# Kernel tuning notes

Hardware: AMD Instinct MI355X
Metric: run time of the kernel (lower is better)

Reference implementation:

```python
import jax, jax.numpy as jnp
import numpy as np

B, C, W, H, HEADS = 8, 512, 32, 32, 8
DH = C // HEADS  # 64
N = W * H        # 1024


def setup_inputs() -> dict:
    key = jax.random.key(0)
    ks = jax.random.split(key, 10)
    s = 1.0 / np.sqrt(C)
    return {
        "x": jax.random.normal(ks[0], (B, C, W, H), jnp.float32),
        "d": jax.random.normal(ks[1], (B, C, W, H), jnp.float32),
        "Wq": jax.random.normal(ks[2], (C, C), jnp.float32) * s,
        "bq": jnp.zeros((C,), jnp.float32),
        "Wk": jax.random.normal(ks[3], (C, C), jnp.float32) * s,
        "bk": jnp.zeros((C,), jnp.float32),
        "Wv": jax.random.normal(ks[4], (C, C), jnp.float32) * s,
        "bv": jnp.zeros((C,), jnp.float32),
        "rel_h": jax.random.normal(ks[5], (1, HEADS, DH, 1, H), jnp.float32),
        "rel_w": jax.random.normal(ks[6], (1, HEADS, DH, W, 1), jnp.float32),
    }


def reference(x, d, Wq, bq, Wk, bk, Wv, bv, rel_h, rel_w):
    b, c, w, h = x.shape
    heads = rel_h.shape[1]
    dh = c // heads
    n = w * h

    def proj(t, Wt, bt):
        # 1x1 conv == per-pixel channel matmul; reshape to [B, heads, dh, N]
        y = jnp.einsum('bchw,oc->bohw', t, Wt) + bt[None, :, None, None]
        return y.reshape(b, heads, dh, n)

    q = proj(x, Wq, bq)
    k = proj(d, Wk, bk)
    v = proj(d, Wv, bv)

    # content-content: q^T k -> [B, h, N, N]
    cc = jnp.einsum('bhdn,bhdm->bhnm', q, k)
    # content-position: (rel_h + rel_w) broadcast -> [1, h, dh, N], then pos^T @ q
    pos = (rel_h + rel_w).reshape(heads, dh, n)
    cp = jnp.einsum('hdm,bhdn->bhmn', pos, q)

    attn = jax.nn.softmax(cc + cp, axis=-1)  # [B, h, N, N]
    # out = v @ attn^T : out[b,h,d,i] = sum_j v[b,h,d,j] * attn[b,h,i,j]
    out = jnp.einsum('bhdj,bhij->bhdi', v, attn)
    return out.reshape(b, c, w, h)
```

## Files before the change

kernel.cpp:

```cpp
#include <hip/hip_runtime.h>

typedef unsigned short u16;
typedef _Float16 f16x8 __attribute__((ext_vector_type(8)));
typedef __fp16 hf16x2 __attribute__((ext_vector_type(2)));
typedef float f32x4 __attribute__((ext_vector_type(4)));
typedef float f32x16 __attribute__((ext_vector_type(16)));
typedef unsigned uint2v __attribute__((ext_vector_type(2)));

#define NB 8
#define NC 512
#define NHD 8
#define DH 64
#define NN 1024
#define LOG2E 1.4426950408889634f

__device__ __forceinline__ u16 f2h(float f) {
    union { _Float16 h; u16 u; } v; v.h = (_Float16)f;
    return v.u;
}

__global__ __launch_bounds__(256) void k_prep(
    const float* __restrict__ x, const float* __restrict__ d,
    const float* __restrict__ Wq, const float* __restrict__ Wk, const float* __restrict__ Wv,
    const float* __restrict__ relh, const float* __restrict__ relw,
    u16* __restrict__ xt, u16* __restrict__ dt,
    u16* __restrict__ wq, u16* __restrict__ wk, u16* __restrict__ wv,
    u16* __restrict__ ps) {
    __shared__ float tile[64][65];
    int id = blockIdx.x, t = threadIdx.x;
    if (id < 2048) {
        int nb = (id & 15) * 64;
        int cb = ((id >> 4) & 7) * 64;
        int z = id >> 7;
        int b = z & 7;
        const float* src = (z >> 3) ? d : x;
        u16* ot = (z >> 3) ? dt : xt;
        {
            int crow = t >> 2, n0 = (t & 3) * 16;
            const float* g = src + ((size_t)(b * NC + cb + crow)) * NN + nb + n0;
#pragma unroll
            for (int k = 0; k < 16; k += 4) {
                float4 v = *(const float4*)(g + k);
                tile[crow][n0 + k + 0] = v.x;
                tile[crow][n0 + k + 1] = v.y;
                tile[crow][n0 + k + 2] = v.z;
                tile[crow][n0 + k + 3] = v.w;
            }
        }
        __syncthreads();
        {
            int nrow = t >> 2, c0 = (t & 3) * 16;
            union { u16 s[16]; uint4 v[2]; } uh;
#pragma unroll
            for (int k = 0; k < 16; ++k) uh.s[k] = f2h(tile[c0 + k][nrow]);
            size_t oidx = ((size_t)(b * NN + nb + nrow)) * NC + cb + c0;
            *(uint4*)(ot + oidx)     = uh.v[0];
            *(uint4*)(ot + oidx + 8) = uh.v[1];
        }
    } else if (id < 2816) {
        int j = id - 2048;
        int m = j >> 8;
        int blk = j & 255;
        const float* src = (m == 0) ? Wq : (m == 1) ? Wk : Wv;
        u16* dst = (m == 0) ? wq : (m == 1) ? wk : wv;
        int i = (blk * 256 + t) * 4;
        float4 v = *(const float4*)(src + i);
        union { u16 s[4]; uint2 u2; } r;
        r.s[0] = f2h(v.x); r.s[1] = f2h(v.y); r.s[2] = f2h(v.z); r.s[3] = f2h(v.w);
        *(uint2*)(dst + i) = r.u2;
    } else {
        int idx = (id - 2816) * 256 + t;
        int dd = idx & 63;
        int i  = (idx >> 6) & 1023;
        int h  = idx >> 16;
        float f = relh[(h * 64 + dd) * 32 + (i & 31)] + relw[(h * 64 + dd) * 32 + (i >> 5)];
        ps[(h * 1024 + i) * 64 + dd] = f2h(f);
    }
}

__global__ __launch_bounds__(256) void k_proj(
    const u16* __restrict__ xt, const u16* __restrict__ dt,
    const u16* __restrict__ wq, const u16* __restrict__ wk, const u16* __restrict__ wv,
    const float* __restrict__ bq, const float* __restrict__ bk, const float* __restrict__ bv,
    u16* __restrict__ qt_o, u16* __restrict__ kt_o, u16* __restrict__ v_o) {
    __shared__ u16 Asm[128 * 32];
    __shared__ u16 Bsm[128 * 32];

    int p = blockIdx.z % 3;
    int b = blockIdx.z / 3;
    const u16 *Ap, *Bp;
    const float* bias;
    u16* Oq;
    if (p == 0)      { Ap = wq; Bp = xt; bias = bq; Oq = qt_o; }
    else if (p == 1) { Ap = wk; Bp = dt; bias = bk; Oq = kt_o; }
    else             { Ap = wv; Bp = dt; bias = bv; Oq = v_o; }
    Bp += (size_t)b * NN * NC;
    float oscale = (p == 0) ? LOG2E : 1.0f;

    int obase = blockIdx.x * 128;
    int nbase = blockIdx.y * 128;
    int t = threadIdx.x, wave = t >> 6, quad = (t & 63) >> 4, l15 = t & 15;
    int wr = (wave >> 1) * 64, wc = (wave & 1) * 64;

    f32x4 acc[4][4];
#pragma unroll
    for (int fo = 0; fo < 4; ++fo)
#pragma unroll
        for (int fn = 0; fn < 4; ++fn)
#pragma unroll
            for (int r = 0; r < 4; ++r) acc[fo][fn][r] = 0.f;

    for (int kk = 0; kk < NC; kk += 32) {
        __syncthreads();
#pragma unroll
        for (int u = 0; u < 2; ++u) {
            int c = u * 256 + t;
            int row = c >> 2, part = c & 3;
            __builtin_amdgcn_global_load_lds(
                (const __attribute__((address_space(1))) void*)(Ap + (size_t)(obase + row) * NC + kk + part * 8),
                (__attribute__((address_space(3))) void*)(Asm + (size_t)(u * 256 + wave * 64) * 8), 16, 0, 0);
            __builtin_amdgcn_global_load_lds(
                (const __attribute__((address_space(1))) void*)(Bp + (size_t)(nbase + row) * NC + kk + part * 8),
                (__attribute__((address_space(3))) void*)(Bsm + (size_t)(u * 256 + wave * 64) * 8), 16, 0, 0);
        }
        __syncthreads();

        f16x8 af[4], bfr[4];
#pragma unroll
        for (int fo = 0; fo < 4; ++fo) af[fo] = *(const f16x8*)&Asm[(wr + fo * 16 + l15) * 32 + quad * 8];
#pragma unroll
        for (int fn = 0; fn < 4; ++fn) bfr[fn] = *(const f16x8*)&Bsm[(wc + fn * 16 + l15) * 32 + quad * 8];
#pragma unroll
        for (int fo = 0; fo < 4; ++fo)
#pragma unroll
            for (int fn = 0; fn < 4; ++fn)
                acc[fo][fn] = __builtin_amdgcn_mfma_f32_16x16x32_f16(af[fo], bfr[fn], acc[fo][fn], 0, 0, 0);
    }

#pragma unroll
    for (int fo = 0; fo < 4; ++fo) {
#pragma unroll
        for (int fn = 0; fn < 4; ++fn) {
            int o0 = obase + wr + fo * 16 + quad * 4;
            int n = nbase + wc + fn * 16 + l15;
            if (p < 2) {
                union { u16 s[4]; uint2 v2; } uh;
#pragma unroll
                for (int r = 0; r < 4; ++r) uh.s[r] = f2h((acc[fo][fn][r] + bias[o0 + r]) * oscale);
                int head = o0 >> 6, dd0 = o0 & 63;
                size_t idx = (((size_t)(b * NHD + head) * NN) + n) * DH + dd0;
                *(uint2*)&Oq[idx] = uh.v2;
            } else {
#pragma unroll
                for (int r = 0; r < 4; ++r) {
                    int o = o0 + r;
                    int head = o >> 6, dd = o & 63;
                    Oq[((size_t)(b * NHD + head) * DH + dd) * NN + n] = f2h(acc[fo][fn][r] + bias[o]);
                }
            }
        }
    }
}

__global__ __launch_bounds__(256, 2) void k_attn(
    const u16* __restrict__ qt, const u16* __restrict__ kt,
    const u16* __restrict__ v_, const u16* __restrict__ pos,
    float* __restrict__ out) {
    __shared__ u16 Bs[128 * 128];
    __shared__ u16 Vt[64 * 128];

    int n = blockIdx.x;
    int g = n & 63;
    int ib = n >> 6;
    int head = g & 7, b = g >> 3;

    int t = threadIdx.x, ws = t >> 6, lane = t & 63, h = lane >> 5, l31 = lane & 31;
    size_t bh = (size_t)(b * NHD + head);
    const u16* qb = qt + bh * NN * DH;
    const u16* kb = kt + bh * NN * DH;
    const u16* vb = v_ + bh * DH * NN;
    const u16* pb = pos + (size_t)head * NN * DH;
    int i0 = ib * 128;
    int iglob = i0 + ws * 32 + l31;

    f16x8 qf[8];
#pragma unroll
    for (int ks = 0; ks < 4; ++ks) qf[ks] = *(const f16x8*)&qb[(size_t)iglob * DH + ks * 16 + h * 8];
#pragma unroll
    for (int ks = 4; ks < 8; ++ks) qf[ks] = *(const f16x8*)&pb[(size_t)iglob * DH + (ks - 4) * 16 + h * 8];

    f32x16 oacc[2];
#pragma unroll
    for (int df = 0; df < 2; ++df)
#pragma unroll
        for (int r = 0; r < 16; ++r) oacc[df][r] = 0.f;
    float m_ = -__builtin_inff(), l_ = 0.f;
    int swz = l31 & 7;

    for (int jc = 0; jc < NN; jc += 128) {
        __syncthreads();
#pragma unroll
        for (int u = 0; u < 8; ++u) {
            int c = u * 256 + t;
            int row = c >> 4, c16 = c & 15;
            int gch = c16 ^ (row & 7);
            const u16* src = (gch < 8) ? &kb[(size_t)(jc + row) * DH + gch * 8]
                                       : &qb[(size_t)(jc + row) * DH + (gch - 8) * 8];
            __builtin_amdgcn_global_load_lds(
                (const __attribute__((address_space(1))) void*)src,
                (__attribute__((address_space(3))) void*)(Bs + (u * 256 + ws * 64) * 8), 16, 0, 0);
        }
#pragma unroll
        for (int u = 0; u < 4; ++u) {
            int c = u * 256 + t;
            int row = c >> 4, c16 = c & 15;
            int gch = c16 ^ (row & 7);
            __builtin_amdgcn_global_load_lds(
                (const __attribute__((address_space(1))) void*)&vb[(size_t)row * NN + jc + gch * 8],
                (__attribute__((address_space(3))) void*)(Vt + (u * 256 + ws * 64) * 8), 16, 0, 0);
        }
        __syncthreads();

        f32x16 sacc[4];
#pragma unroll
        for (int jf = 0; jf < 4; ++jf)
#pragma unroll
            for (int r = 0; r < 16; ++r) sacc[jf][r] = 0.f;
        __builtin_amdgcn_s_setprio(1);
#pragma unroll
        for (int jf = 0; jf < 4; ++jf)
#pragma unroll
            for (int ks = 0; ks < 8; ++ks) {
                f16x8 af = *(const f16x8*)&Bs[(jf * 32 + l31) * 128 + ((ks * 2 + h) ^ swz) * 8];
                sacc[jf] = __builtin_amdgcn_mfma_f32_32x32x16_f16(af, qf[ks], sacc[jf], 0, 0, 0);
            }
        __builtin_amdgcn_s_setprio(0);

        float mj[4];
#pragma unroll
        for (int jf = 0; jf < 4; ++jf) {
            float a = fmaxf(fmaxf(sacc[jf][0], sacc[jf][1]), sacc[jf][2]);
            a = fmaxf(fmaxf(a, sacc[jf][3]), sacc[jf][4]);
            a = fmaxf(fmaxf(a, sacc[jf][5]), sacc[jf][6]);
            a = fmaxf(fmaxf(a, sacc[jf][7]), sacc[jf][8]);
            a = fmaxf(fmaxf(a, sacc[jf][9]), sacc[jf][10]);
            a = fmaxf(fmaxf(a, sacc[jf][11]), sacc[jf][12]);
            a = fmaxf(fmaxf(a, sacc[jf][13]), sacc[jf][14]);
            mj[jf] = fmaxf(a, sacc[jf][15]);
        }
        float mloc = fmaxf(fmaxf(mj[0], mj[1]), fmaxf(mj[2], mj[3]));
        mloc = fmaxf(mloc, __shfl_xor(mloc, 32));
        if (__any(mloc - m_ > 8.f)) {
            float mnew = fmaxf(m_, mloc);
            float alpha = __builtin_amdgcn_exp2f(m_ - mnew);
            m_ = mnew;
#pragma unroll
            for (int df = 0; df < 2; ++df)
#pragma unroll
                for (int r = 0; r < 16; ++r) oacc[df][r] *= alpha;
            l_ *= alpha;
        }
        float ls[4];
#pragma unroll
        for (int jf = 0; jf < 4; ++jf) {
            float s = 0.f;
#pragma unroll
            for (int r = 0; r < 16; ++r) {
                float pv = __builtin_amdgcn_exp2f(sacc[jf][r] - m_);
                sacc[jf][r] = pv;
                s += pv;
            }
            ls[jf] = s;
        }
        float lsum = (ls[0] + ls[1]) + (ls[2] + ls[3]);
        lsum += __shfl_xor(lsum, 32);
        l_ += lsum;

        __builtin_amdgcn_s_setprio(1);
#pragma unroll
        for (int jw = 0; jw < 8; ++jw) {
            int jf = jw >> 1, r0 = (jw & 1) * 8;
            union { hf16x2 v; unsigned u; } a0, a1, b0, b1;
            a0.v = __builtin_amdgcn_cvt_pkrtz(sacc[jf][r0 + 0], sacc[jf][r0 + 1]);
            a1.v = __builtin_amdgcn_cvt_pkrtz(sacc[jf][r0 + 2], sacc[jf][r0 + 3]);
            b0.v = __builtin_amdgcn_cvt_pkrtz(sacc[jf][r0 + 4], sacc[jf][r0 + 5]);
            b1.v = __builtin_amdgcn_cvt_pkrtz(sacc[jf][r0 + 6], sacc[jf][r0 + 7]);
            uint2v s0 = __builtin_amdgcn_permlane32_swap(a0.u, b0.u, false, false);
            uint2v s1 = __builtin_amdgcn_permlane32_swap(a1.u, b1.u, false, false);
            union { unsigned w[4]; f16x8 f; } pf;
            pf.w[0] = s0.x;
            pf.w[1] = s1.x;
            pf.w[2] = s0.y;
            pf.w[3] = s1.y;
#pragma unroll
            for (int df = 0; df < 2; ++df) {
                f16x8 vf = *(const f16x8*)&Vt[(df * 32 + l31) * 128 + ((jw * 2 + h) ^ swz) * 8];
                oacc[df] = __builtin_amdgcn_mfma_f32_32x32x16_f16(vf, pf.f, oacc[df], 0, 0, 0);
            }
        }
        __builtin_amdgcn_s_setprio(0);
    }

    float li = 1.0f / l_;
#pragma unroll
    for (int df = 0; df < 2; ++df)
#pragma unroll
        for (int r = 0; r < 16; ++r) {
            int dd = df * 32 + (r & 3) + 8 * (r >> 2) + 4 * h;
            out[((size_t)(b * NC) + head * DH + dd) * NN + i0 + ws * 32 + l31] = oacc[df][r] * li;
        }
}

#define SXT  (8u * 1024u * 512u * 2u)
#define SW   (512u * 512u * 2u)
#define SQT  SXT
#define SPOS (8u * 1024u * 64u * 2u)

#define OFF_XT   (0u)
#define OFF_DT   (OFF_XT + SXT)
#define OFF_WQ   (OFF_DT + SXT)
#define OFF_WK   (OFF_WQ + SW)
#define OFF_WV   (OFF_WK + SW)
#define OFF_QT   (OFF_WV + SW)
#define OFF_KT   (OFF_QT + SQT)
#define OFF_V    (OFF_KT + SQT)
#define OFF_POS  (OFF_V + SQT)

extern "C" void kernel_launch(void* const* d_in, const int* in_sizes, int n_in,
                              void* d_out, int out_size, void* d_ws, size_t ws_size,
                              hipStream_t stream) {
    const float* x   = (const float*)d_in[0];
    const float* d   = (const float*)d_in[1];
    const float* Wq  = (const float*)d_in[2];
    const float* bq  = (const float*)d_in[3];
    const float* Wk  = (const float*)d_in[4];
    const float* bk  = (const float*)d_in[5];
    const float* Wv  = (const float*)d_in[6];
    const float* bv  = (const float*)d_in[7];
    const float* rh  = (const float*)d_in[8];
    const float* rw  = (const float*)d_in[9];

    char* ws = (char*)d_ws;
    u16* xt = (u16*)(ws + OFF_XT);
    u16* dt = (u16*)(ws + OFF_DT);
    u16* wq = (u16*)(ws + OFF_WQ);
    u16* wk = (u16*)(ws + OFF_WK);
    u16* wv = (u16*)(ws + OFF_WV);
    u16* qt = (u16*)(ws + OFF_QT);
    u16* kt = (u16*)(ws + OFF_KT);
    u16* v_ = (u16*)(ws + OFF_V);
    u16* ps = (u16*)(ws + OFF_POS);

    k_prep<<<4864, 256, 0, stream>>>(x, d, Wq, Wk, Wv, rh, rw, xt, dt, wq, wk, wv, ps);
    k_proj<<<dim3(4, 8, 24), 256, 0, stream>>>(xt, dt, wq, wk, wv, bq, bk, bv, qt, kt, v_);
    k_attn<<<512, 256, 0, stream>>>(qt, kt, v_, ps, (float*)d_out);
}
```

Baseline: 164.8 us.

## Double-buffer LDS tiles in projection and attention kernels

Both the projection GEMM and the attention kernel now use two LDS buffers. Each iteration issues the async global-to-LDS loads for the next tile before computing on the current one, and synchronises once at the end of the iteration instead of twice. To keep the LDS budget unchanged, the attention key/value chunk shrinks from 128 to 64 columns, which doubles the number of softmax and rescale steps per row block. The goal is to hide global load latency behind MFMA work, at the cost of more loop overhead and more online-softmax bookkeeping.

```diff
diff --git a/kernel.cpp b/kernel.cpp
--- a/kernel.cpp
+++ b/kernel.cpp
@@ -83,8 +83,8 @@
     const u16* __restrict__ wq, const u16* __restrict__ wk, const u16* __restrict__ wv,
     const float* __restrict__ bq, const float* __restrict__ bk, const float* __restrict__ bv,
     u16* __restrict__ qt_o, u16* __restrict__ kt_o, u16* __restrict__ v_o) {
-    __shared__ u16 Asm[128 * 32];
-    __shared__ u16 Bsm[128 * 32];
+    __shared__ u16 Asm[2][128 * 32];
+    __shared__ u16 Bsm[2][128 * 32];
 
     int p = blockIdx.z % 3;
     int b = blockIdx.z / 3;
@@ -110,31 +110,39 @@
 #pragma unroll
             for (int r = 0; r < 4; ++r) acc[fo][fn][r] = 0.f;
 
-    for (int kk = 0; kk < NC; kk += 32) {
-        __syncthreads();
+    auto stage = [&](int kk, int buf) {
 #pragma unroll
         for (int u = 0; u < 2; ++u) {
             int c = u * 256 + t;
             int row = c >> 2, part = c & 3;
             __builtin_amdgcn_global_load_lds(
                 (const __attribute__((address_space(1))) void*)(Ap + (size_t)(obase + row) * NC + kk + part * 8),
-                (__attribute__((address_space(3))) void*)(Asm + (size_t)(u * 256 + wave * 64) * 8), 16, 0, 0);
+                (__attribute__((address_space(3))) void*)(&Asm[buf][0] + (size_t)(u * 256 + wave * 64) * 8), 16, 0, 0);
             __builtin_amdgcn_global_load_lds(
                 (const __attribute__((address_space(1))) void*)(Bp + (size_t)(nbase + row) * NC + kk + part * 8),
-                (__attribute__((address_space(3))) void*)(Bsm + (size_t)(u * 256 + wave * 64) * 8), 16, 0, 0);
-        }
-        __syncthreads();
+                (__attribute__((address_space(3))) void*)(&Bsm[buf][0] + (size_t)(u * 256 + wave * 64) * 8), 16, 0, 0);
+        }
+    };
+
+    stage(0, 0);
+    __syncthreads();
+
+    for (int kk = 0; kk < NC; kk += 32) {
+        int cur = (kk >> 5) & 1;
+        if (kk + 32 < NC) stage(kk + 32, cur ^ 1);
 
         f16x8 af[4], bfr[4];
 #pragma unroll
-        for (int fo = 0; fo < 4; ++fo) af[fo] = *(const f16x8*)&Asm[(wr + fo * 16 + l15) * 32 + quad * 8];
-#pragma unroll
-        for (int fn = 0; fn < 4; ++fn) bfr[fn] = *(const f16x8*)&Bsm[(wc + fn * 16 + l15) * 32 + quad * 8];
+        for (int fo = 0; fo < 4; ++fo) af[fo] = *(const f16x8*)&Asm[cur][(wr + fo * 16 + l15) * 32 + quad * 8];
+#pragma unroll
+        for (int fn = 0; fn < 4; ++fn) bfr[fn] = *(const f16x8*)&Bsm[cur][(wc + fn * 16 + l15) * 32 + quad * 8];
 #pragma unroll
         for (int fo = 0; fo < 4; ++fo)
 #pragma unroll
             for (int fn = 0; fn < 4; ++fn)
                 acc[fo][fn] = __builtin_amdgcn_mfma_f32_16x16x32_f16(af[fo], bfr[fn], acc[fo][fn], 0, 0, 0);
+
+        __syncthreads();
     }
 
 #pragma unroll
@@ -166,8 +174,8 @@
     const u16* __restrict__ qt, const u16* __restrict__ kt,
     const u16* __restrict__ v_, const u16* __restrict__ pos,
     float* __restrict__ out) {
-    __shared__ u16 Bs[128 * 128];
-    __shared__ u16 Vt[64 * 128];
+    __shared__ u16 Bs[2][64 * 128];
+    __shared__ u16 Vt[2][64 * 64];
 
     int n = blockIdx.x;
     int g = n & 63;
@@ -197,10 +205,9 @@
     float m_ = -__builtin_inff(), l_ = 0.f;
     int swz = l31 & 7;
 
-    for (int jc = 0; jc < NN; jc += 128) {
-        __syncthreads();
-#pragma unroll
-        for (int u = 0; u < 8; ++u) {
+    auto stage = [&](int jc, int buf) {
+#pragma unroll
+        for (int u = 0; u < 4; ++u) {
             int c = u * 256 + t;
             int row = c >> 4, c16 = c & 15;
             int gch = c16 ^ (row & 7);
@@ -208,37 +215,44 @@
                                        : &qb[(size_t)(jc + row) * DH + (gch - 8) * 8];
             __builtin_amdgcn_global_load_lds(
                 (const __attribute__((address_space(1))) void*)src,
-                (__attribute__((address_space(3))) void*)(Bs + (u * 256 + ws * 64) * 8), 16, 0, 0);
-        }
-#pragma unroll
-        for (int u = 0; u < 4; ++u) {
+                (__attribute__((address_space(3))) void*)(&Bs[buf][0] + (u * 256 + ws * 64) * 8), 16, 0, 0);
+        }
+#pragma unroll
+        for (int u = 0; u < 2; ++u) {
             int c = u * 256 + t;
-            int row = c >> 4, c16 = c & 15;
-            int gch = c16 ^ (row & 7);
+            int row = c >> 3, c8 = c & 7;
+            int gch = c8 ^ (row & 7);
             __builtin_amdgcn_global_load_lds(
                 (const __attribute__((address_space(1))) void*)&vb[(size_t)row * NN + jc + gch * 8],
-                (__attribute__((address_space(3))) void*)(Vt + (u * 256 + ws * 64) * 8), 16, 0, 0);
-        }
-        __syncthreads();
-
-        f32x16 sacc[4];
-#pragma unroll
-        for (int jf = 0; jf < 4; ++jf)
+                (__attribute__((address_space(3))) void*)(&Vt[buf][0] + (u * 256 + ws * 64) * 8), 16, 0, 0);
+        }
+    };
+
+    stage(0, 0);
+    __syncthreads();
+
+    for (int it = 0; it < 16; ++it) {
+        int cur = it & 1;
+        if (it < 15) stage((it + 1) * 64, cur ^ 1);
+
+        f32x16 sacc[2];
+#pragma unroll
+        for (int jf = 0; jf < 2; ++jf)
 #pragma unroll
             for (int r = 0; r < 16; ++r) sacc[jf][r] = 0.f;
         __builtin_amdgcn_s_setprio(1);
 #pragma unroll
-        for (int jf = 0; jf < 4; ++jf)
+        for (int jf = 0; jf < 2; ++jf)
 #pragma unroll
             for (int ks = 0; ks < 8; ++ks) {
-                f16x8 af = *(const f16x8*)&Bs[(jf * 32 + l31) * 128 + ((ks * 2 + h) ^ swz) * 8];
+                f16x8 af = *(const f16x8*)&Bs[cur][(jf * 32 + l31) * 128 + ((ks * 2 + h) ^ swz) * 8];
                 sacc[jf] = __builtin_amdgcn_mfma_f32_32x32x16_f16(af, qf[ks], sacc[jf], 0, 0, 0);
             }
         __builtin_amdgcn_s_setprio(0);
 
-        float mj[4];
-#pragma unroll
-        for (int jf = 0; jf < 4; ++jf) {
+        float mj[2];
+#pragma unroll
+        for (int jf = 0; jf < 2; ++jf) {
             float a = fmaxf(fmaxf(sacc[jf][0], sacc[jf][1]), sacc[jf][2]);
             a = fmaxf(fmaxf(a, sacc[jf][3]), sacc[jf][4]);
             a = fmaxf(fmaxf(a, sacc[jf][5]), sacc[jf][6]);
@@ -248,7 +262,7 @@
             a = fmaxf(fmaxf(a, sacc[jf][13]), sacc[jf][14]);
             mj[jf] = fmaxf(a, sacc[jf][15]);
         }
-        float mloc = fmaxf(fmaxf(mj[0], mj[1]), fmaxf(mj[2], mj[3]));
+        float mloc = fmaxf(mj[0], mj[1]);
         mloc = fmaxf(mloc, __shfl_xor(mloc, 32));
         if (__any(mloc - m_ > 8.f)) {
             float mnew = fmaxf(m_, mloc);
@@ -260,9 +274,9 @@
                 for (int r = 0; r < 16; ++r) oacc[df][r] *= alpha;
             l_ *= alpha;
         }
-        float ls[4];
-#pragma unroll
-        for (int jf = 0; jf < 4; ++jf) {
+        float ls[2];
+#pragma unroll
+        for (int jf = 0; jf < 2; ++jf) {
             float s = 0.f;
 #pragma unroll
             for (int r = 0; r < 16; ++r) {
@@ -272,13 +286,13 @@
             }
             ls[jf] = s;
         }
-        float lsum = (ls[0] + ls[1]) + (ls[2] + ls[3]);
+        float lsum = ls[0] + ls[1];
         lsum += __shfl_xor(lsum, 32);
         l_ += lsum;
 
         __builtin_amdgcn_s_setprio(1);
 #pragma unroll
-        for (int jw = 0; jw < 8; ++jw) {
+        for (int jw = 0; jw < 4; ++jw) {
             int jf = jw >> 1, r0 = (jw & 1) * 8;
             union { hf16x2 v; unsigned u; } a0, a1, b0, b1;
             a0.v = __builtin_amdgcn_cvt_pkrtz(sacc[jf][r0 + 0], sacc[jf][r0 + 1]);
@@ -294,11 +308,13 @@
             pf.w[3] = s1.y;
 #pragma unroll
             for (int df = 0; df < 2; ++df) {
-                f16x8 vf = *(const f16x8*)&Vt[(df * 32 + l31) * 128 + ((jw * 2 + h) ^ swz) * 8];
+                f16x8 vf = *(const f16x8*)&Vt[cur][(df * 32 + l31) * 64 + ((jw * 2 + h) ^ swz) * 8];
                 oacc[df] = __builtin_amdgcn_mfma_f32_32x32x16_f16(vf, pf.f, oacc[df], 0, 0, 0);
             }
         }
         __builtin_amdgcn_s_setprio(0);
+
+        __syncthreads();
     }
 
     float li = 1.0f / l_;
```

Result: faster. 157.8 us (-4.2%).

## Double-buffer LDS tiles in projection and attention kernels to overlap loads

Applied to the files above, without the earlier changes.

The projection GEMM gets double-buffered A/B LDS tiles, so the next K-slice is issued via global_load_lds before the current slice's MFMAs run. The attention kernel double-buffers the V tile and issues the next K/Q tile load into the single Bs buffer after the score stage finishes, so it overlaps the PV MFMAs. The aim is to hide global-to-LDS latency behind compute. In exchange, LDS use grows, which may affect occupancy in k_attn (launch_bounds 256,2), and correctness depends on the async LDS loads being complete at each barrier.

```diff
diff --git a/kernel.cpp b/kernel.cpp
--- a/kernel.cpp
+++ b/kernel.cpp
@@ -83,8 +83,8 @@
     const u16* __restrict__ wq, const u16* __restrict__ wk, const u16* __restrict__ wv,
     const float* __restrict__ bq, const float* __restrict__ bk, const float* __restrict__ bv,
     u16* __restrict__ qt_o, u16* __restrict__ kt_o, u16* __restrict__ v_o) {
-    __shared__ u16 Asm[128 * 32];
-    __shared__ u16 Bsm[128 * 32];
+    __shared__ u16 Asm[2][128 * 32];
+    __shared__ u16 Bsm[2][128 * 32];
 
     int p = blockIdx.z % 3;
     int b = blockIdx.z / 3;
@@ -110,31 +110,39 @@
 #pragma unroll
             for (int r = 0; r < 4; ++r) acc[fo][fn][r] = 0.f;
 
-    for (int kk = 0; kk < NC; kk += 32) {
-        __syncthreads();
+    auto stage = [&](int kk, int buf) {
 #pragma unroll
         for (int u = 0; u < 2; ++u) {
             int c = u * 256 + t;
             int row = c >> 2, part = c & 3;
             __builtin_amdgcn_global_load_lds(
                 (const __attribute__((address_space(1))) void*)(Ap + (size_t)(obase + row) * NC + kk + part * 8),
-                (__attribute__((address_space(3))) void*)(Asm + (size_t)(u * 256 + wave * 64) * 8), 16, 0, 0);
+                (__attribute__((address_space(3))) void*)(&Asm[buf][0] + (size_t)(u * 256 + wave * 64) * 8), 16, 0, 0);
             __builtin_amdgcn_global_load_lds(
                 (const __attribute__((address_space(1))) void*)(Bp + (size_t)(nbase + row) * NC + kk + part * 8),
-                (__attribute__((address_space(3))) void*)(Bsm + (size_t)(u * 256 + wave * 64) * 8), 16, 0, 0);
-        }
-        __syncthreads();
+                (__attribute__((address_space(3))) void*)(&Bsm[buf][0] + (size_t)(u * 256 + wave * 64) * 8), 16, 0, 0);
+        }
+    };
+
+    stage(0, 0);
+    __syncthreads();
+
+    for (int kk = 0; kk < NC; kk += 32) {
+        int cur = (kk >> 5) & 1;
+        if (kk + 32 < NC) stage(kk + 32, cur ^ 1);
 
         f16x8 af[4], bfr[4];
 #pragma unroll
-        for (int fo = 0; fo < 4; ++fo) af[fo] = *(const f16x8*)&Asm[(wr + fo * 16 + l15) * 32 + quad * 8];
-#pragma unroll
-        for (int fn = 0; fn < 4; ++fn) bfr[fn] = *(const f16x8*)&Bsm[(wc + fn * 16 + l15) * 32 + quad * 8];
+        for (int fo = 0; fo < 4; ++fo) af[fo] = *(const f16x8*)&Asm[cur][(wr + fo * 16 + l15) * 32 + quad * 8];
+#pragma unroll
+        for (int fn = 0; fn < 4; ++fn) bfr[fn] = *(const f16x8*)&Bsm[cur][(wc + fn * 16 + l15) * 32 + quad * 8];
 #pragma unroll
         for (int fo = 0; fo < 4; ++fo)
 #pragma unroll
             for (int fn = 0; fn < 4; ++fn)
                 acc[fo][fn] = __builtin_amdgcn_mfma_f32_16x16x32_f16(af[fo], bfr[fn], acc[fo][fn], 0, 0, 0);
+
+        __syncthreads();
     }
 
 #pragma unroll
@@ -167,7 +175,7 @@
     const u16* __restrict__ v_, const u16* __restrict__ pos,
     float* __restrict__ out) {
     __shared__ u16 Bs[128 * 128];
-    __shared__ u16 Vt[64 * 128];
+    __shared__ u16 Vt[2][64 * 128];
 
     int n = blockIdx.x;
     int g = n & 63;
@@ -197,8 +205,7 @@
     float m_ = -__builtin_inff(), l_ = 0.f;
     int swz = l31 & 7;
 
-    for (int jc = 0; jc < NN; jc += 128) {
-        __syncthreads();
+    auto stageB = [&](int jc) {
 #pragma unroll
         for (int u = 0; u < 8; ++u) {
             int c = u * 256 + t;
@@ -210,6 +217,8 @@
                 (const __attribute__((address_space(1))) void*)src,
                 (__attribute__((address_space(3))) void*)(Bs + (u * 256 + ws * 64) * 8), 16, 0, 0);
         }
+    };
+    auto stageV = [&](int jc, int buf) {
 #pragma unroll
         for (int u = 0; u < 4; ++u) {
             int c = u * 256 + t;
@@ -217,9 +226,17 @@
             int gch = c16 ^ (row & 7);
             __builtin_amdgcn_global_load_lds(
                 (const __attribute__((address_space(1))) void*)&vb[(size_t)row * NN + jc + gch * 8],
-                (__attribute__((address_space(3))) void*)(Vt + (u * 256 + ws * 64) * 8), 16, 0, 0);
-        }
-        __syncthreads();
+                (__attribute__((address_space(3))) void*)(&Vt[buf][0] + (u * 256 + ws * 64) * 8), 16, 0, 0);
+        }
+    };
+
+    stageB(0);
+    stageV(0, 0);
+    __syncthreads();
+
+    for (int it = 0; it < 8; ++it) {
+        int cur = it & 1;
+        if (it < 7) stageV((it + 1) * 128, cur ^ 1);
 
         f32x16 sacc[4];
 #pragma unroll
@@ -275,6 +292,9 @@
         float lsum = (ls[0] + ls[1]) + (ls[2] + ls[3]);
         lsum += __shfl_xor(lsum, 32);
         l_ += lsum;
+
+        __syncthreads();
+        if (it < 7) stageB((it + 1) * 128);
 
         __builtin_amdgcn_s_setprio(1);
 #pragma unroll
@@ -294,11 +314,13 @@
             pf.w[3] = s1.y;
 #pragma unroll
             for (int df = 0; df < 2; ++df) {
-                f16x8 vf = *(const f16x8*)&Vt[(df * 32 + l31) * 128 + ((jw * 2 + h) ^ swz) * 8];
+                f16x8 vf = *(const f16x8*)&Vt[cur][(df * 32 + l31) * 128 + ((jw * 2 + h) ^ swz) * 8];
                 oacc[df] = __builtin_amdgcn_mfma_f32_32x32x16_f16(vf, pf.f, oacc[df], 0, 0, 0);
             }
         }
         __builtin_amdgcn_s_setprio(0);
+
+        __syncthreads();
     }
 
     float li = 1.0f / l_;
```

Measured after the change: 157.9 us. -4.1%, faster.
